# Performance work log

Measured on AMD Instinct MI355X. Metric: run time of the kernel, lower is better.

The kernel has to match this reference:

```python
import jax, jax.numpy as jnp
import numpy as np

NUM_HEADS = 3
WIN = 7            # window_size (square)
PAD = WIN // 2     # conv / v padding


def setup_inputs() -> dict:
    key = jax.random.key(0)
    ks = jax.random.split(key, 8)
    B, C, H, W = 8, 96, 56, 56
    hd = C // NUM_HEADS  # 32
    x = jax.random.normal(ks[0], (B, C, H, W), jnp.float32)
    # qkv 1x1 conv: weight (3C, C), bias (3C,)
    w_qkv = jax.random.normal(ks[1], (3 * C, C), jnp.float32) * (C ** -0.5)
    b_qkv = jax.random.normal(ks[2], (3 * C,), jnp.float32) * 0.01
    fan_in = 2 * hd * WIN * WIN
    w_dm = jax.random.normal(ks[3], (WIN * WIN, 2 * hd, WIN, WIN), jnp.float32) * (fan_in ** -0.5)
    b_dm = jax.random.normal(ks[4], (WIN * WIN,), jnp.float32) * 0.01
    bias_table = jax.random.normal(ks[5], (WIN * WIN, NUM_HEADS), jnp.float32) * 0.02
    # proj 1x1 conv
    w_proj = jax.random.normal(ks[6], (C, C), jnp.float32) * (C ** -0.5)
    b_proj = jax.random.normal(ks[7], (C,), jnp.float32) * 0.01
    return dict(x=x, w_qkv=w_qkv, b_qkv=b_qkv, w_dm=w_dm, b_dm=b_dm,
                bias_table=bias_table, w_proj=w_proj, b_proj=b_proj)


def reference(x, w_qkv, b_qkv, w_dm, b_dm, bias_table, w_proj, b_proj):
    B, C, H, W = x.shape
    nh = NUM_HEADS
    hd = C // nh
    scale = hd ** -0.5

    # qkv 1x1 conv -> (B, 3, nh, hd, H, W)
    qkv = jnp.einsum('oc,bchw->bohw', w_qkv, x) + b_qkv[None, :, None, None]
    qkv = qkv.reshape(B, 3, nh, hd, H, W)
    q, k, v = qkv[:, 0], qkv[:, 1], qkv[:, 2]

    qk = jnp.concatenate([(q * scale).reshape(B * nh, hd, H, W),
                          k.reshape(B * nh, hd, H, W)], axis=1)
    attn = jax.lax.conv_general_dilated(
        qk, w_dm, window_strides=(1, 1), padding=[(PAD, PAD), (PAD, PAD)],
        dimension_numbers=('NCHW', 'OIHW', 'NCHW')) + b_dm[None, :, None, None]
    attn = attn.reshape(B, nh, WIN * WIN, H, W)

    # relative position bias, broadcast over spatial dims
    attn = attn + bias_table.T.reshape(1, nh, WIN * WIN, 1, 1)
    attn = jax.nn.softmax(attn, axis=2)

    # gather sliding windows of v from a zero-padded tensor
    v_pad = jnp.pad(v, ((0, 0), (0, 0), (0, 0), (PAD, PAD), (PAD, PAD)))
    vw = jnp.stack([v_pad[..., i // WIN:i // WIN + H, i % WIN:i % WIN + W]
                    for i in range(WIN * WIN)], axis=3)

    # weighted sum over window dim, merge heads back to channels
    out = jnp.sum(vw * attn[:, :, None], axis=3).reshape(B, C, H, W)

    # output 1x1 projection (dropout p=0 -> identity)
    out = jnp.einsum('oc,bchw->bohw', w_proj, out) + b_proj[None, :, None, None]
    return out
```

## Files before the change

kernel.cpp:

```cpp
#include <hip/hip_runtime.h>
#include <hip/hip_bf16.h>
#include <stdint.h>

#define BATCH 8
#define CCH 96
#define NH 3
#define HD 32
#define HGT 56
#define WID 56
#define HW 3136
#define WIN 7
#define KK 49
#define PADR 3
#define NIMG 24
#define C2 64

typedef const float* fp32p;
typedef __attribute__((ext_vector_type(8))) short bf16x8;
typedef __attribute__((ext_vector_type(16))) float f32x16;
typedef unsigned short ushort_t;

__device__ __forceinline__ float bf2f_bits(unsigned u){ return __uint_as_float(u << 16); }
__device__ __forceinline__ ushort_t f2bf_bits(float f){
  __hip_bfloat16 hb = __float2bfloat16(f);
  return *(ushort_t*)&hb;
}

__global__ void prep_kernel(fp32p w_dm, fp32p b_dm, fp32p bias_table,
                            fp32p w_qkv, fp32p w_proj,
                            __hip_bfloat16* __restrict__ w3, float* __restrict__ bias3,
                            ushort_t* __restrict__ wq3, ushort_t* __restrict__ wp3){
  int t = blockIdx.x * 256 + threadIdx.x;
  if (t < 200704){
    int j   = t & 7;
    int l   = (t >> 3) & 63;
    int mt  = (t >> 9) & 1;
    int cb  = (t >> 10) & 1;
    int pt  = t >> 11;
    int pass = pt / KK, tap = pt % KK;
    int o  = mt*32 + (l & 31);
    int ch = pass*32 + cb*16 + (l >> 5)*8 + j;
    float v = 0.f;
    if (o < KK) v = w_dm[((size_t)(o*C2 + ch))*KK + tap];
    w3[t] = __float2bfloat16(v);
  } else if (t < 200896){
    int t2 = t - 200704;
    int h = t2 >> 6;
    int o = t2 & 63;
    bias3[t2] = (o < KK) ? (b_dm[o] + bias_table[o*NH + h]) : -1e30f;
  } else if (t < 200896 + 27648){
    int i = t - 200896;
    int j = i & 7, l = (i >> 3) & 63;
    int rest = i >> 9;
    int mt = rest % 9, k = rest / 9;
    int o = mt*32 + (l & 31);
    int c = k*16 + (l >> 5)*8 + j;
    wq3[i] = f2bf_bits(w_qkv[o*CCH + c]);
  } else if (t < 200896 + 27648 + 9216){
    int i = t - 200896 - 27648;
    int j = i & 7, l = (i >> 3) & 63;
    int rest = i >> 9;
    int mt = rest % 3, k = rest / 3;
    int o = mt*32 + (l & 31);
    int c = k*16 + (l >> 5)*8 + j;
    wp3[i] = f2bf_bits(w_proj[o*CCH + c]);
  }
}

__global__ __launch_bounds__(256) void xt_kernel(fp32p x, ushort_t* __restrict__ xbf){
  __shared__ float lds[128*97];
  int px0 = blockIdx.x * 128;
  int tid = threadIdx.x;
  #pragma unroll
  for (int it = 0; it < 48; ++it){
    int s = tid + it*256;
    int px = s & 127;
    int c  = s >> 7;
    int gpx = px0 + px;
    int b = gpx / HW, pp = gpx % HW;
    lds[px*97 + c] = x[((size_t)b*CCH + c)*HW + pp];
  }
  __syncthreads();
  #pragma unroll
  for (int it = 0; it < 6; ++it){
    int s = tid + it*256;
    int j  = s % 12;
    int px = s / 12;
    unsigned u[4];
    #pragma unroll
    for (int q = 0; q < 4; ++q){
      float f0 = lds[px*97 + j*8 + 2*q];
      float f1 = lds[px*97 + j*8 + 2*q + 1];
      u[q] = (unsigned)f2bf_bits(f0) | ((unsigned)f2bf_bits(f1) << 16);
    }
    uint4 w4; w4.x=u[0]; w4.y=u[1]; w4.z=u[2]; w4.w=u[3];
    *(uint4*)((char*)xbf + ((size_t)(px0+px)*96 + j*8)*2) = w4;
  }
}

__global__ __launch_bounds__(64) void qkv_kernel(const ushort_t* __restrict__ xbf,
    const ushort_t* __restrict__ wq3, fp32p b_qkv,
    ushort_t* __restrict__ qplane, ushort_t* __restrict__ kplane,
    ushort_t* __restrict__ v2){
  int wid = blockIdx.x;
  int g  = wid / 784;
  int pt = wid % 784;
  int l = threadIdx.x & 63, col = l & 31, hi = l >> 5;
  int px = pt*32 + col;
  int b = px / HW, pp = px % HW;

  bf16x8 B[6];
  const char* bb = (const char*)xbf + (size_t)px*192 + hi*16;
  #pragma unroll
  for (int k = 0; k < 6; ++k) B[k] = *(const bf16x8*)(bb + k*32);

  f32x16 acc[3];
  #pragma unroll
  for (int m = 0; m < 3; ++m)
    #pragma unroll
    for (int r = 0; r < 16; ++r) acc[m][r] = 0.f;

  #pragma unroll
  for (int k = 0; k < 6; ++k){
    #pragma unroll
    for (int m = 0; m < 3; ++m){
      bf16x8 A = *(const bf16x8*)((const char*)wq3 + ((size_t)((k*9 + g*3 + m)*64 + l))*16);
      acc[m] = __builtin_amdgcn_mfma_f32_32x32x16_bf16(A, B[k], acc[m], 0, 0, 0);
    }
  }
  const float scale = 0.17677669529663687f;
  ushort_t* plane = (g == 0) ? qplane : (g == 1 ? kplane : v2);
  #pragma unroll
  for (int m = 0; m < 3; ++m){
    ushort_t* dst = plane + ((size_t)((b*NH + m)*HW + pp))*32;
    #pragma unroll
    for (int q = 0; q < 4; ++q){
      int base = 8*q + 4*hi;
      float v0 = acc[m][q*4+0] + b_qkv[g*96 + m*32 + base + 0];
      float v1 = acc[m][q*4+1] + b_qkv[g*96 + m*32 + base + 1];
      float v2f = acc[m][q*4+2] + b_qkv[g*96 + m*32 + base + 2];
      float v3 = acc[m][q*4+3] + b_qkv[g*96 + m*32 + base + 3];
      if (g == 0){ v0 *= scale; v1 *= scale; v2f *= scale; v3 *= scale; }
      uint2 pk;
      pk.x = (unsigned)f2bf_bits(v0) | ((unsigned)f2bf_bits(v1) << 16);
      pk.y = (unsigned)f2bf_bits(v2f) | ((unsigned)f2bf_bits(v3) << 16);
      *(uint2*)(&dst[base]) = pk;
    }
  }
}

#define MFMA4K(Ab, Bb) \
  { _Pragma("unroll") for (int nt = 0; nt < 2; ++nt){ \
      acc[0][nt] = __builtin_amdgcn_mfma_f32_32x32x16_bf16(Ab[0], Bb[nt], acc[0][nt], 0, 0, 0); \
      acc[1][nt] = __builtin_amdgcn_mfma_f32_32x32x16_bf16(Ab[1], Bb[nt], acc[1][nt], 0, 0, 0); \
    } }

#define LOADAK(tt, Ab) \
  { const char* An_ = Abase + (size_t)(tt)*4096; \
    Ab[0] = *(const bf16x8*)(An_); \
    Ab[1] = *(const bf16x8*)(An_ + 1024); }

#define LOADBK(tt, Bb) \
  { int ky_ = (tt) / 7, kx_ = (tt) - ky_*7; \
    _Pragma("unroll") for (int nt = 0; nt < 2; ++nt){ \
      int xp_ = nt*32 + col + kx_; if (xp_ > 61) xp_ = 61; \
      int base_ = ((row + ky_)*64 + xp_)*64; \
      int sx_ = (xp_ & 3) ^ ((xp_ >> 2) & 3); \
      Bb[nt] = *(const bf16x8*)(&smem[base_ + ((((cbw << 1) | hi) ^ sx_) << 4)]); } }

#define XWRITE(A0v, A1v) \
  { _Pragma("unroll") for (int q = 0; q < 4; ++q){ \
      float4 v4; \
      v4.x=A0v[4*q+0]; v4.y=A0v[4*q+1]; v4.z=A0v[4*q+2]; v4.w=A0v[4*q+3]; \
      *(float4*)((char*)xch + slot_o*256 + (((2*q+hi) ^ xsw)<<4)) = v4; \
      v4.x=A1v[4*q+0]; v4.y=A1v[4*q+1]; v4.z=A1v[4*q+2]; v4.w=A1v[4*q+3]; \
      *(float4*)((char*)xch + slot_o*256 + (((8+2*q+hi) ^ xsw)<<4)) = v4; } }

#define XREAD(A0v, A1v) \
  { _Pragma("unroll") for (int q = 0; q < 4; ++q){ \
      float4 v4 = *(const float4*)((char*)xch + slot_s*256 + (((2*q+hi) ^ xsw)<<4)); \
      A0v[4*q+0]+=v4.x; A0v[4*q+1]+=v4.y; A0v[4*q+2]+=v4.z; A0v[4*q+3]+=v4.w; \
      v4 = *(const float4*)((char*)xch + slot_s*256 + (((8+2*q+hi) ^ xsw)<<4)); \
      A1v[4*q+0]+=v4.x; A1v[4*q+1]+=v4.y; A1v[4*q+2]+=v4.z; A1v[4*q+3]+=v4.w; } }

__global__ __launch_bounds__(256, 3) void attn_kernel(
    const ushort_t* __restrict__ qplane, const ushort_t* __restrict__ kplane,
    const __hip_bfloat16* __restrict__ w3, const float* __restrict__ bias3,
    const ushort_t* __restrict__ v2, ushort_t* __restrict__ tmp2){
  __shared__ char smem[50176];

  int bid = blockIdx.x;
  int n  = bid / 28;
  int y0 = (bid % 28) * 2;
  int b = n / NH, head = n % NH;
  int tid = threadIdx.x;
  int l = tid & 63, w = tid >> 6, hi = l >> 5, col = l & 31;
  int row = w >> 1;
  int cbw = w & 1;

  f32x16 acc[2][2];
  #pragma unroll
  for (int r = 0; r < 16; ++r){
    int rowv = (r & 3) + 8*(r >> 2) + 4*hi;
    float b0 = (cbw == 0) ? bias3[head*64 + rowv] : 0.f;
    float b1 = (cbw == 0) ? bias3[head*64 + 32 + rowv] : 0.f;
    #pragma unroll
    for (int nt = 0; nt < 2; ++nt){ acc[0][nt][r] = b0; acc[1][nt][r] = b1; }
  }

  for (int pass = 0; pass < 2; ++pass){
    if (pass) __syncthreads();
    const char* src = (const char*)(pass ? kplane : qplane) + (size_t)n * HW * 64;
    #pragma unroll
    for (int it = 0; it < 8; ++it){
      int s = tid + it*256;
      int c   = s & 3;
      int xp  = (s >> 2) & 63;
      int rw  = s >> 8;
      int gy = y0 - 3 + rw;
      int gx = xp - 3;
      uint4 val = {0,0,0,0};
      if ((unsigned)gy < HGT && (unsigned)gx < WID)
        val = *(const uint4*)(src + (size_t)(gy*WID + gx)*64 + c*16);
      int sw = (c ^ (xp & 3) ^ ((xp >> 2) & 3)) << 4;
      *(uint4*)(&smem[(rw*64 + xp)*64 + sw]) = val;
    }
    __syncthreads();

    const char* Abase = (const char*)w3 + (size_t)pass*KK*4096 + cbw*2048 + l*16;
    bf16x8 A0[2], A1[2], B0[2], B1[2];
    LOADAK(0, A0); LOADBK(0, B0);
    LOADAK(1, A1); LOADBK(1, B1);
    for (int t = 0; t < 48; t += 2){
      MFMA4K(A0, B0);
      LOADAK(t+2, A0); LOADBK(t+2, B0);
      MFMA4K(A1, B1);
      int t3 = (t+3 < KK) ? (t+3) : 48;
      LOADAK(t3, A1); LOADBK(t3, B1);
    }
    MFMA4K(A0, B0);
  }

  __syncthreads();
  float* xch = (float*)smem;
  int xsw = col & 15;
  {
    int slot_o = row*64 + (1-cbw)*32 + col;
    if (cbw == 0){ XWRITE(acc[0][1], acc[1][1]); }
    else         { XWRITE(acc[0][0], acc[1][0]); }
  }
  __syncthreads();
  f32x16 a0, a1;
  {
    int slot_s = row*64 + cbw*32 + col;
    if (cbw == 0){ XREAD(acc[0][0], acc[1][0]); a0 = acc[0][0]; a1 = acc[1][0]; }
    else         { XREAD(acc[0][1], acc[1][1]); a0 = acc[0][1]; a1 = acc[1][1]; }
  }

  const char* vb = (const char*)v2 + (size_t)n * HW * 64;
  uint4 vreg[8];
  #pragma unroll
  for (int it = 0; it < 8; ++it){
    int s = tid + it*256;
    int xp  = s & 63;
    int c   = (s >> 6) & 3;
    int rw  = s >> 8;
    int gy = y0 - 3 + rw;
    int gx = xp - 3;
    uint4 val = {0,0,0,0};
    if ((unsigned)gy < HGT && (unsigned)gx < WID)
      val = *(const uint4*)(vb + (size_t)(gy*WID + gx)*64 + c*16);
    vreg[it] = val;
  }

  ushort_t* Pp = (ushort_t*)&smem[32768];
  {
    float m = -1e30f;
    #pragma unroll
    for (int r = 0; r < 16; ++r){ m = fmaxf(m, a0[r]); m = fmaxf(m, a1[r]); }
    m = fmaxf(m, __shfl_xor(m, 32));
    float s = 0.f;
    #pragma unroll
    for (int r = 0; r < 16; ++r){
      a0[r] = __expf(a0[r] - m); s += a0[r];
      a1[r] = __expf(a1[r] - m); s += a1[r];
    }
    s += __shfl_xor(s, 32);
    float inv = 1.f / s;
    int pixslot = row*64 + cbw*32 + col;
    ushort_t* Pr = Pp + pixslot*68;
    #pragma unroll
    for (int q = 0; q < 4; ++q){
      int base = 8*q + 4*hi;
      uint2 pk0;
      pk0.x = (unsigned)f2bf_bits(a0[q*4+0]*inv) | ((unsigned)f2bf_bits(a0[q*4+1]*inv) << 16);
      pk0.y = (unsigned)f2bf_bits(a0[q*4+2]*inv) | ((unsigned)f2bf_bits(a0[q*4+3]*inv) << 16);
      *(uint2*)(&Pr[base]) = pk0;
      uint2 pk1;
      pk1.x = (unsigned)f2bf_bits(a1[q*4+0]*inv) | ((unsigned)f2bf_bits(a1[q*4+1]*inv) << 16);
      pk1.y = (unsigned)f2bf_bits(a1[q*4+2]*inv) | ((unsigned)f2bf_bits(a1[q*4+3]*inv) << 16);
      *(uint2*)(&Pr[32 + base]) = pk1;
    }
  }
  __syncthreads();

  #pragma unroll
  for (int it = 0; it < 8; ++it){
    int s = tid + it*256;
    int xp  = s & 63;
    int c   = (s >> 6) & 3;
    int rw  = s >> 8;
    *(uint4*)(&smem[((c*8 + rw)*64 + xp)*16]) = vreg[it];
  }
  __syncthreads();

  int ch2 = tid >> 7;
  int slot = tid & 127;
  int pr = slot >> 6, pxx = slot & 63;
  if (pxx < WID){
    float out[16];
    #pragma unroll
    for (int i = 0; i < 16; ++i) out[i] = 0.f;
    #pragma unroll
    for (int ky = 0; ky < WIN; ++ky){
      #pragma unroll
      for (int kx = 0; kx < WIN; ++kx){
        float pw = bf2f_bits(Pp[slot*68 + ky*7 + kx]);
        int vrow = pr + ky, xp = pxx + kx;
        #pragma unroll
        for (int ci = 0; ci < 2; ++ci){
          int cc = ch2*2 + ci;
          uint4 vv = *(const uint4*)(&smem[((cc*8 + vrow)*64 + xp)*16]);
          unsigned ua[4] = {vv.x, vv.y, vv.z, vv.w};
          #pragma unroll
          for (int q = 0; q < 4; ++q){
            out[ci*8 + 2*q]     = fmaf(pw, __uint_as_float(ua[q] << 16),         out[ci*8 + 2*q]);
            out[ci*8 + 2*q + 1] = fmaf(pw, __uint_as_float(ua[q] & 0xffff0000u), out[ci*8 + 2*q + 1]);
          }
        }
      }
    }
    int pp = (y0 + pr)*WID + pxx;
    ushort_t* dst = tmp2 + ((size_t)(b*HW + pp))*96 + head*32 + ch2*16;
    #pragma unroll
    for (int j2 = 0; j2 < 2; ++j2){
      unsigned u[4];
      #pragma unroll
      for (int q = 0; q < 4; ++q){
        u[q] = (unsigned)f2bf_bits(out[j2*8 + 2*q]) | ((unsigned)f2bf_bits(out[j2*8 + 2*q + 1]) << 16);
      }
      uint4 w4; w4.x=u[0]; w4.y=u[1]; w4.z=u[2]; w4.w=u[3];
      *(uint4*)(&dst[j2*8]) = w4;
    }
  }
}

__global__ __launch_bounds__(64) void proj_kernel(const ushort_t* __restrict__ tmp2,
    const ushort_t* __restrict__ wp3, fp32p b_proj, float* __restrict__ outp){
  int pt = blockIdx.x;
  int l = threadIdx.x & 63, col = l & 31, hi = l >> 5;
  int px = pt*32 + col;
  int b = px / HW, pp = px % HW;

  bf16x8 B[6];
  const char* bb = (const char*)tmp2 + (size_t)px*192 + hi*16;
  #pragma unroll
  for (int k = 0; k < 6; ++k) B[k] = *(const bf16x8*)(bb + k*32);

  f32x16 acc[3];
  #pragma unroll
  for (int m = 0; m < 3; ++m)
    #pragma unroll
    for (int r = 0; r < 16; ++r) acc[m][r] = 0.f;

  #pragma unroll
  for (int k = 0; k < 6; ++k){
    #pragma unroll
    for (int m = 0; m < 3; ++m){
      bf16x8 A = *(const bf16x8*)((const char*)wp3 + ((size_t)((k*3 + m)*64 + l))*16);
      acc[m] = __builtin_amdgcn_mfma_f32_32x32x16_bf16(A, B[k], acc[m], 0, 0, 0);
    }
  }
  #pragma unroll
  for (int m = 0; m < 3; ++m){
    #pragma unroll
    for (int r = 0; r < 16; ++r){
      int o = m*32 + (r & 3) + 8*(r >> 2) + 4*hi;
      outp[((size_t)(b*CCH + o))*HW + pp] = acc[m][r] + b_proj[o];
    }
  }
}

extern "C" void kernel_launch(void* const* d_in, const int* in_sizes, int n_in,
                              void* d_out, int out_size, void* d_ws, size_t ws_size,
                              hipStream_t stream){
  fp32p x          = (fp32p)d_in[0];
  fp32p w_qkv      = (fp32p)d_in[1];
  fp32p b_qkv      = (fp32p)d_in[2];
  fp32p w_dm       = (fp32p)d_in[3];
  fp32p b_dm       = (fp32p)d_in[4];
  fp32p bias_table = (fp32p)d_in[5];
  fp32p w_proj     = (fp32p)d_in[6];
  fp32p b_proj     = (fp32p)d_in[7];

  char* ws = (char*)d_ws;
  const size_t XBF_BYTES   = (size_t)BATCH * HW * 96 * 2;
  const size_t PLANE_BYTES = (size_t)NIMG * HW * 32 * 2;
  const size_t TMP2_BYTES  = (size_t)BATCH * HW * 96 * 2;
  const size_t W3_BYTES    = 200704ull * 2;
  size_t off = 0;
  ushort_t* xbf    = (ushort_t*)(ws + off); off += XBF_BYTES;
  ushort_t* qplane = (ushort_t*)(ws + off); off += PLANE_BYTES;
  ushort_t* kplane = (ushort_t*)(ws + off); off += PLANE_BYTES;
  ushort_t* v2     = (ushort_t*)(ws + off); off += PLANE_BYTES;
  ushort_t* tmp2   = (ushort_t*)(ws + off); off += TMP2_BYTES;
  __hip_bfloat16* w3 = (__hip_bfloat16*)(ws + off); off += W3_BYTES;
  float* bias3     = (float*)(ws + off);    off += 192*4;
  ushort_t* wq3    = (ushort_t*)(ws + off); off += 27648*2;
  ushort_t* wp3    = (ushort_t*)(ws + off); off += 9216*2;

  hipLaunchKernelGGL(prep_kernel, dim3(929), dim3(256), 0, stream,
                     w_dm, b_dm, bias_table, w_qkv, w_proj, w3, bias3, wq3, wp3);
  hipLaunchKernelGGL(xt_kernel, dim3(196), dim3(256), 0, stream, x, xbf);
  hipLaunchKernelGGL(qkv_kernel, dim3(2352), dim3(64), 0, stream,
                     xbf, wq3, b_qkv, qplane, kplane, v2);
  hipLaunchKernelGGL(attn_kernel, dim3(672), dim3(256), 0, stream,
                     qplane, kplane, w3, bias3, v2, tmp2);
  hipLaunchKernelGGL(proj_kernel, dim3(784), dim3(64), 0, stream,
                     tmp2, wp3, b_proj, (float*)d_out);
}
```

Measured before the change: 78.04 us.

## Merge prep and transpose kernels, remap attn block order, pack FMAs

Merges the weight-prep kernel and the x-transpose kernel into one launch, with the block index choosing which job a block does, which removes one kernel launch and the gap after it. Remaps attn_kernel block IDs with an 8-way interleave so that neighbouring dispatched blocks work on different images, presumably to spread them across XCDs and their L2 caches. Rewrites the V-weighted accumulation with two-wide float vectors so the compiler can emit packed FMA instructions. Risks: the merged kernel's prep blocks now reserve the 50 KB LDS array they never use, which can lower occupancy, and the remap may reduce cache reuse of neighbouring rows.

Result: faster. 74.47 us (-4.6%).

```diff
diff --git a/kernel.cpp b/kernel.cpp
--- a/kernel.cpp
+++ b/kernel.cpp
@@ -18,6 +18,7 @@
 typedef const float* fp32p;
 typedef __attribute__((ext_vector_type(8))) short bf16x8;
 typedef __attribute__((ext_vector_type(16))) float f32x16;
+typedef __attribute__((ext_vector_type(2))) float f32x2;
 typedef unsigned short ushort_t;
 
 __device__ __forceinline__ float bf2f_bits(unsigned u){ return __uint_as_float(u << 16); }
@@ -26,75 +27,77 @@
   return *(ushort_t*)&hb;
 }
 
-__global__ void prep_kernel(fp32p w_dm, fp32p b_dm, fp32p bias_table,
-                            fp32p w_qkv, fp32p w_proj,
-                            __hip_bfloat16* __restrict__ w3, float* __restrict__ bias3,
-                            ushort_t* __restrict__ wq3, ushort_t* __restrict__ wp3){
-  int t = blockIdx.x * 256 + threadIdx.x;
-  if (t < 200704){
-    int j   = t & 7;
-    int l   = (t >> 3) & 63;
-    int mt  = (t >> 9) & 1;
-    int cb  = (t >> 10) & 1;
-    int pt  = t >> 11;
-    int pass = pt / KK, tap = pt % KK;
-    int o  = mt*32 + (l & 31);
-    int ch = pass*32 + cb*16 + (l >> 5)*8 + j;
-    float v = 0.f;
-    if (o < KK) v = w_dm[((size_t)(o*C2 + ch))*KK + tap];
-    w3[t] = __float2bfloat16(v);
-  } else if (t < 200896){
-    int t2 = t - 200704;
-    int h = t2 >> 6;
-    int o = t2 & 63;
-    bias3[t2] = (o < KK) ? (b_dm[o] + bias_table[o*NH + h]) : -1e30f;
-  } else if (t < 200896 + 27648){
-    int i = t - 200896;
-    int j = i & 7, l = (i >> 3) & 63;
-    int rest = i >> 9;
-    int mt = rest % 9, k = rest / 9;
-    int o = mt*32 + (l & 31);
-    int c = k*16 + (l >> 5)*8 + j;
-    wq3[i] = f2bf_bits(w_qkv[o*CCH + c]);
-  } else if (t < 200896 + 27648 + 9216){
-    int i = t - 200896 - 27648;
-    int j = i & 7, l = (i >> 3) & 63;
-    int rest = i >> 9;
-    int mt = rest % 3, k = rest / 3;
-    int o = mt*32 + (l & 31);
-    int c = k*16 + (l >> 5)*8 + j;
-    wp3[i] = f2bf_bits(w_proj[o*CCH + c]);
-  }
-}
-
-__global__ __launch_bounds__(256) void xt_kernel(fp32p x, ushort_t* __restrict__ xbf){
+__global__ __launch_bounds__(256) void prep_xt_kernel(fp32p w_dm, fp32p b_dm,
+    fp32p bias_table, fp32p w_qkv, fp32p w_proj, fp32p x,
+    __hip_bfloat16* __restrict__ w3, float* __restrict__ bias3,
+    ushort_t* __restrict__ wq3, ushort_t* __restrict__ wp3,
+    ushort_t* __restrict__ xbf){
   __shared__ float lds[128*97];
-  int px0 = blockIdx.x * 128;
-  int tid = threadIdx.x;
-  #pragma unroll
-  for (int it = 0; it < 48; ++it){
-    int s = tid + it*256;
-    int px = s & 127;
-    int c  = s >> 7;
-    int gpx = px0 + px;
-    int b = gpx / HW, pp = gpx % HW;
-    lds[px*97 + c] = x[((size_t)b*CCH + c)*HW + pp];
-  }
-  __syncthreads();
-  #pragma unroll
-  for (int it = 0; it < 6; ++it){
-    int s = tid + it*256;
-    int j  = s % 12;
-    int px = s / 12;
-    unsigned u[4];
-    #pragma unroll
-    for (int q = 0; q < 4; ++q){
-      float f0 = lds[px*97 + j*8 + 2*q];
-      float f1 = lds[px*97 + j*8 + 2*q + 1];
-      u[q] = (unsigned)f2bf_bits(f0) | ((unsigned)f2bf_bits(f1) << 16);
-    }
-    uint4 w4; w4.x=u[0]; w4.y=u[1]; w4.z=u[2]; w4.w=u[3];
-    *(uint4*)((char*)xbf + ((size_t)(px0+px)*96 + j*8)*2) = w4;
+  int bx = blockIdx.x;
+  if (bx < 929){
+    int t = bx * 256 + threadIdx.x;
+    if (t < 200704){
+      int j   = t & 7;
+      int l   = (t >> 3) & 63;
+      int mt  = (t >> 9) & 1;
+      int cb  = (t >> 10) & 1;
+      int pt  = t >> 11;
+      int pass = pt / KK, tap = pt % KK;
+      int o  = mt*32 + (l & 31);
+      int ch = pass*32 + cb*16 + (l >> 5)*8 + j;
+      float v = 0.f;
+      if (o < KK) v = w_dm[((size_t)(o*C2 + ch))*KK + tap];
+      w3[t] = __float2bfloat16(v);
+    } else if (t < 200896){
+      int t2 = t - 200704;
+      int h = t2 >> 6;
+      int o = t2 & 63;
+      bias3[t2] = (o < KK) ? (b_dm[o] + bias_table[o*NH + h]) : -1e30f;
+    } else if (t < 200896 + 27648){
+      int i = t - 200896;
+      int j = i & 7, l = (i >> 3) & 63;
+      int rest = i >> 9;
+      int mt = rest % 9, k = rest / 9;
+      int o = mt*32 + (l & 31);
+      int c = k*16 + (l >> 5)*8 + j;
+      wq3[i] = f2bf_bits(w_qkv[o*CCH + c]);
+    } else if (t < 200896 + 27648 + 9216){
+      int i = t - 200896 - 27648;
+      int j = i & 7, l = (i >> 3) & 63;
+      int rest = i >> 9;
+      int mt = rest % 3, k = rest / 3;
+      int o = mt*32 + (l & 31);
+      int c = k*16 + (l >> 5)*8 + j;
+      wp3[i] = f2bf_bits(w_proj[o*CCH + c]);
+    }
+  } else {
+    int px0 = (bx - 929) * 128;
+    int tid = threadIdx.x;
+    #pragma unroll
+    for (int it = 0; it < 48; ++it){
+      int s = tid + it*256;
+      int px = s & 127;
+      int c  = s >> 7;
+      int gpx = px0 + px;
+      int b = gpx / HW, pp = gpx % HW;
+      lds[px*97 + c] = x[((size_t)b*CCH + c)*HW + pp];
+    }
+    __syncthreads();
+    #pragma unroll
+    for (int it = 0; it < 6; ++it){
+      int s = tid + it*256;
+      int j  = s % 12;
+      int px = s / 12;
+      unsigned u[4];
+      #pragma unroll
+      for (int q = 0; q < 4; ++q){
+        float f0 = lds[px*97 + j*8 + 2*q];
+        float f1 = lds[px*97 + j*8 + 2*q + 1];
+        u[q] = (unsigned)f2bf_bits(f0) | ((unsigned)f2bf_bits(f1) << 16);
+      }
+      uint4 w4; w4.x=u[0]; w4.y=u[1]; w4.z=u[2]; w4.w=u[3];
+      *(uint4*)((char*)xbf + ((size_t)(px0+px)*96 + j*8)*2) = w4;
+    }
   }
 }
 
@@ -189,7 +192,8 @@
     const ushort_t* __restrict__ v2, ushort_t* __restrict__ tmp2){
   __shared__ char smem[50176];
 
-  int bid = blockIdx.x;
+  int d = blockIdx.x;
+  int bid = (d & 7)*84 + (d >> 3);
   int n  = bid / 28;
   int y0 = (bid % 28) * 2;
   int b = n / NH, head = n % NH;
@@ -318,14 +322,15 @@
   int slot = tid & 127;
   int pr = slot >> 6, pxx = slot & 63;
   if (pxx < WID){
-    float out[16];
-    #pragma unroll
-    for (int i = 0; i < 16; ++i) out[i] = 0.f;
+    f32x2 out2[8];
+    #pragma unroll
+    for (int i = 0; i < 8; ++i){ out2[i].x = 0.f; out2[i].y = 0.f; }
     #pragma unroll
     for (int ky = 0; ky < WIN; ++ky){
       #pragma unroll
       for (int kx = 0; kx < WIN; ++kx){
         float pw = bf2f_bits(Pp[slot*68 + ky*7 + kx]);
+        f32x2 pw2; pw2.x = pw; pw2.y = pw;
         int vrow = pr + ky, xp = pxx + kx;
         #pragma unroll
         for (int ci = 0; ci < 2; ++ci){
@@ -334,8 +339,10 @@
           unsigned ua[4] = {vv.x, vv.y, vv.z, vv.w};
           #pragma unroll
           for (int q = 0; q < 4; ++q){
-            out[ci*8 + 2*q]     = fmaf(pw, __uint_as_float(ua[q] << 16),         out[ci*8 + 2*q]);
-            out[ci*8 + 2*q + 1] = fmaf(pw, __uint_as_float(ua[q] & 0xffff0000u), out[ci*8 + 2*q + 1]);
+            f32x2 v2f;
+            v2f.x = __uint_as_float(ua[q] << 16);
+            v2f.y = __uint_as_float(ua[q] & 0xffff0000u);
+            out2[ci*4 + q] += pw2 * v2f;
           }
         }
       }
@@ -347,7 +354,7 @@
       unsigned u[4];
       #pragma unroll
       for (int q = 0; q < 4; ++q){
-        u[q] = (unsigned)f2bf_bits(out[j2*8 + 2*q]) | ((unsigned)f2bf_bits(out[j2*8 + 2*q + 1]) << 16);
+        u[q] = (unsigned)f2bf_bits(out2[j2*4 + q].x) | ((unsigned)f2bf_bits(out2[j2*4 + q].y) << 16);
       }
       uint4 w4; w4.x=u[0]; w4.y=u[1]; w4.z=u[2]; w4.w=u[3];
       *(uint4*)(&dst[j2*8]) = w4;
@@ -419,9 +426,9 @@
   ushort_t* wq3    = (ushort_t*)(ws + off); off += 27648*2;
   ushort_t* wp3    = (ushort_t*)(ws + off); off += 9216*2;
 
-  hipLaunchKernelGGL(prep_kernel, dim3(929), dim3(256), 0, stream,
-                     w_dm, b_dm, bias_table, w_qkv, w_proj, w3, bias3, wq3, wp3);
-  hipLaunchKernelGGL(xt_kernel, dim3(196), dim3(256), 0, stream, x, xbf);
+  hipLaunchKernelGGL(prep_xt_kernel, dim3(1125), dim3(256), 0, stream,
+                     w_dm, b_dm, bias_table, w_qkv, w_proj, x,
+                     w3, bias3, wq3, wp3, xbf);
   hipLaunchKernelGGL(qkv_kernel, dim3(2352), dim3(64), 0, stream,
                      xbf, wq3, b_qkv, qplane, kplane, v2);
   hipLaunchKernelGGL(attn_kernel, dim3(672), dim3(256), 0, stream,
```
